# Performance work log

Measured on AMD Instinct MI355X. Metric: run time of the kernel, lower is better.

## Reference

```python
import jax, jax.numpy as jnp
import numpy as np

EPS = 1e-12  # guard sqrt at zero


def setup_inputs() -> dict:
    key = jax.random.key(0)
    k1, k2, k3 = jax.random.split(key, 3)
    B, N = 16, 2048
    pred_points = jax.random.normal(k1, (B, N, 3), dtype=jnp.float32)
    target_points = jax.random.normal(k2, (B, N, 3), dtype=jnp.float32)
    # binary symmetry flag per object, kept float for the blend
    sym_flag = (jax.random.uniform(k3, (B,)) > 0.5).astype(jnp.float32)
    return {"pred_points": pred_points, "target_points": target_points, "sym_flag": sym_flag}


def reference(pred_points, target_points, sym_flag):
    # Chamfer (ADD-S style): per pred point, min Euclidean distance to any target point.
    # Pairwise squared distances via ||p||^2 + ||t||^2 - 2 p.t  -> [B, N, M]
    p2 = jnp.sum(pred_points * pred_points, axis=-1)[:, :, None]   # [B,N,1]
    t2 = jnp.sum(target_points * target_points, axis=-1)[:, None, :]  # [B,1,M]
    cross = jnp.einsum('bnd,bmd->bnm', pred_points, target_points)  # [B,N,M]
    d2 = p2 + t2 - 2.0 * cross
    dist = jnp.sqrt(jnp.maximum(d2, EPS))                           # [B,N,M]
    sym_dis = jnp.min(dist, axis=2).mean(axis=1)                    # [B]

    # L2 (ADD style): per-point correspondence distance.
    asym_dis = jnp.linalg.norm(pred_points - target_points, axis=2).mean(axis=1)  # [B]

    all_loss = sym_flag * sym_dis + (1.0 - sym_flag) * asym_dis
    return all_loss.mean()
```

## Files before the change

### kernel.cpp

```cpp
#include <hip/hip_runtime.h>
#include <hip/hip_bf16.h>
#include <math.h>


typedef short short8 __attribute__((ext_vector_type(8)));
typedef float f32x16 __attribute__((ext_vector_type(16)));

__device__ __forceinline__ unsigned short f2bf(float f) {
  unsigned u = __float_as_uint(f);
  u = u + 0x7FFFu + ((u >> 16) & 1u);
  return (unsigned short)(u >> 16);
}
__device__ __forceinline__ float bf2f(unsigned short h) {
  return __uint_as_float(((unsigned)h) << 16);
}

#define TPB 256
#define NPTS 2048

__global__ __launch_bounds__(TPB, 2) void chamfer_main_kernel(
    const float* __restrict__ pred, const float* __restrict__ targ,
    const float* __restrict__ sym_flag, float* __restrict__ partial,
    int N, int B, int panelsPerBatch) {
  __shared__ short8 sA[2][NPTS];
  __shared__ float sm[4][64];

  const int blk = blockIdx.x;
  const int pp = blk % panelsPerBatch;
  const int b = blk / panelsPerBatch;

  const float* tb = targ + (size_t)b * N * 3;
  for (int t = threadIdx.x; t < NPTS; t += TPB) {
    const float x = tb[t * 3], y = tb[t * 3 + 1], z = tb[t * 3 + 2];
    const unsigned short thx = f2bf(x), thy = f2bf(y), thz = f2bf(z);
    const unsigned short tlx = f2bf(x - bf2f(thx));
    const unsigned short tly = f2bf(y - bf2f(thy));
    const unsigned short tlz = f2bf(z - bf2f(thz));
    const float q = 0.5f * (x * x + y * y + z * z);
    const unsigned short qh = f2bf(q), ql = f2bf(q - bf2f(qh));
    sA[0][t] = short8{(short)thx, (short)thy, (short)thz, (short)thx,
                      (short)thy, (short)thz, (short)tlx, (short)tly};
    sA[1][t] = short8{(short)tlz, (short)qh, (short)ql, 0, 0, 0, 0, 0};
  }

  const int lane = threadIdx.x & 63;
  const int w = threadIdx.x >> 6;
  const int g = lane >> 5;
  const int l31 = lane & 31;
  const int colBase = pp * 64;

  short8 bf0, bf1;
#pragma unroll
  for (int pt = 0; pt < 2; ++pt) {
    const int col = colBase + pt * 32 + l31;
    const float* pq = pred + ((size_t)b * N + col) * 3;
    const float x = pq[0], y = pq[1], z = pq[2];
    const unsigned short hx = f2bf(-x), hy = f2bf(-y), hz = f2bf(-z);
    const unsigned short lx = f2bf(-x - bf2f(hx));
    const unsigned short ly = f2bf(-y - bf2f(hy));
    const unsigned short lz = f2bf(-z - bf2f(hz));
    short8 r;
    if (g == 0)
      r = short8{(short)hx, (short)hy, (short)hz, (short)lx,
                 (short)ly, (short)lz, (short)hx, (short)hy};
    else
      r = short8{(short)hz, (short)0x3F80, (short)0x3F80, 0, 0, 0, 0, 0};
    if (pt == 0) bf0 = r; else bf1 = r;
  }
  __syncthreads();

  const f32x16 zc = {0.f, 0.f, 0.f, 0.f, 0.f, 0.f, 0.f, 0.f,
                     0.f, 0.f, 0.f, 0.f, 0.f, 0.f, 0.f, 0.f};
  float rm0[8], rm1[8];
#pragma unroll
  for (int i = 0; i < 8; ++i) { rm0[i] = 3.4e38f; rm1[i] = 3.4e38f; }

#pragma unroll 4
  for (int ta = 0; ta < 16; ++ta) {
    const short8 a = sA[g][w * 512 + ta * 32 + l31];
    const f32x16 d0 = __builtin_amdgcn_mfma_f32_32x32x16_bf16(a, bf0, zc, 0, 0, 0);
    const f32x16 d1 = __builtin_amdgcn_mfma_f32_32x32x16_bf16(a, bf1, zc, 0, 0, 0);
#pragma unroll
    for (int i = 0; i < 8; ++i) {
      rm0[i] = fminf(rm0[i], fminf(d0[2 * i], d0[2 * i + 1]));
      rm1[i] = fminf(rm1[i], fminf(d1[2 * i], d1[2 * i + 1]));
    }
  }

  float m0 = rm0[0], m1 = rm1[0];
#pragma unroll
  for (int i = 1; i < 8; ++i) { m0 = fminf(m0, rm0[i]); m1 = fminf(m1, rm1[i]); }
  m0 = fminf(m0, __shfl_xor(m0, 32));
  m1 = fminf(m1, __shfl_xor(m1, 32));
  if (lane < 32) {
    sm[w][l31] = m0;
    sm[w][32 + l31] = m1;
  }
  __syncthreads();

  if (threadIdx.x < 64) {
    const int i = threadIdx.x;
    const float mm = fminf(fminf(sm[0][i], sm[1][i]), fminf(sm[2][i], sm[3][i]));
    const size_t gc = (size_t)b * N + colBase + i;
    const float x = pred[gc * 3], y = pred[gc * 3 + 1], z = pred[gc * 3 + 2];
    const float tx = targ[gc * 3], ty = targ[gc * 3 + 1], tz = targ[gc * 3 + 2];
    const float hp2 = 0.5f * (x * x + y * y + z * z);
    const float dsym = sqrtf(fmaxf(2.f * (mm + hp2), 1e-12f));
    const float dx = x - tx, dy = y - ty, dz = z - tz;
    const float dasym = sqrtf(dx * dx + dy * dy + dz * dz);
    const float f = sym_flag[b];
    float c = f * dsym + (1.f - f) * dasym;
#pragma unroll
    for (int off = 32; off > 0; off >>= 1) c += __shfl_xor(c, off);
    if (i == 0) partial[blk] = c;
  }
}

__global__ __launch_bounds__(256) void chamfer_sum_kernel(
    const float* __restrict__ partial, float* __restrict__ out, float invNB) {
  const int t = threadIdx.x;
  float s = partial[t] + partial[t + 256];
#pragma unroll
  for (int off = 32; off > 0; off >>= 1) s += __shfl_xor(s, off);
  __shared__ float sW[4];
  if ((t & 63) == 0) sW[t >> 6] = s;
  __syncthreads();
  if (t == 0) out[0] = (sW[0] + sW[1] + sW[2] + sW[3]) * invNB;
}

extern "C" void kernel_launch(void* const* d_in, const int* in_sizes, int n_in,
                              void* d_out, int out_size, void* d_ws, size_t ws_size,
                              hipStream_t stream) {
  const float* pred = (const float*)d_in[0];
  const float* targ = (const float*)d_in[1];
  const float* sym_flag = (const float*)d_in[2];
  float* out = (float*)d_out;

  const int B = in_sizes[2];
  const int N = in_sizes[0] / (B * 3);

  const int panelsPerBatch = N / 64;
  const int grid = B * panelsPerBatch;
  float* partial = (float*)d_ws;

  chamfer_main_kernel<<<grid, TPB, 0, stream>>>(pred, targ, sym_flag, partial,
                                                N, B, panelsPerBatch);
  chamfer_sum_kernel<<<1, 256, 0, stream>>>(partial, out,
                                            1.0f / (float)(N * B));
}
```

Measured before the change: 14.86 us.

## Stage target points per wave with vector loads and drop the block barrier

Each wave now loads and converts only the 512 target points it later consumes, using float4 global loads of eight points per lane. This removes the block-wide __syncthreads between staging and the MFMA loop. The second shared-memory half is shrunk from short8 to short4, cutting LDS use from about 64KB to about 48KB. In exchange, the inner loop has a half-wave branch between the two LDS arrays plus vector repacking, and correctness relies on each wave reading only the region it wrote.

```diff
diff --git a/kernel.cpp b/kernel.cpp
--- a/kernel.cpp
+++ b/kernel.cpp
@@ -4,6 +4,7 @@
 
 
 typedef short short8 __attribute__((ext_vector_type(8)));
+typedef short short4v __attribute__((ext_vector_type(4)));
 typedef float f32x16 __attribute__((ext_vector_type(16)));
 
 __device__ __forceinline__ unsigned short f2bf(float f) {
@@ -22,26 +23,13 @@
     const float* __restrict__ pred, const float* __restrict__ targ,
     const float* __restrict__ sym_flag, float* __restrict__ partial,
     int N, int B, int panelsPerBatch) {
-  __shared__ short8 sA[2][NPTS];
+  __shared__ short8 sA0[NPTS];
+  __shared__ short4v sA1[NPTS];
   __shared__ float sm[4][64];
 
   const int blk = blockIdx.x;
   const int pp = blk % panelsPerBatch;
   const int b = blk / panelsPerBatch;
-
-  const float* tb = targ + (size_t)b * N * 3;
-  for (int t = threadIdx.x; t < NPTS; t += TPB) {
-    const float x = tb[t * 3], y = tb[t * 3 + 1], z = tb[t * 3 + 2];
-    const unsigned short thx = f2bf(x), thy = f2bf(y), thz = f2bf(z);
-    const unsigned short tlx = f2bf(x - bf2f(thx));
-    const unsigned short tly = f2bf(y - bf2f(thy));
-    const unsigned short tlz = f2bf(z - bf2f(thz));
-    const float q = 0.5f * (x * x + y * y + z * z);
-    const unsigned short qh = f2bf(q), ql = f2bf(q - bf2f(qh));
-    sA[0][t] = short8{(short)thx, (short)thy, (short)thz, (short)thx,
-                      (short)thy, (short)thz, (short)tlx, (short)tly};
-    sA[1][t] = short8{(short)tlz, (short)qh, (short)ql, 0, 0, 0, 0, 0};
-  }
 
   const int lane = threadIdx.x & 63;
   const int w = threadIdx.x >> 6;
@@ -67,7 +55,31 @@
       r = short8{(short)hz, (short)0x3F80, (short)0x3F80, 0, 0, 0, 0, 0};
     if (pt == 0) bf0 = r; else bf1 = r;
   }
-  __syncthreads();
+
+  {
+    const int t0 = w * 512 + lane * 8;
+    const float4* tg4 = (const float4*)(targ + ((size_t)b * N + t0) * 3);
+    float tf[24];
+#pragma unroll
+    for (int k = 0; k < 6; ++k) {
+      const float4 v = tg4[k];
+      tf[4 * k] = v.x; tf[4 * k + 1] = v.y;
+      tf[4 * k + 2] = v.z; tf[4 * k + 3] = v.w;
+    }
+#pragma unroll
+    for (int j = 0; j < 8; ++j) {
+      const float x = tf[3 * j], y = tf[3 * j + 1], z = tf[3 * j + 2];
+      const unsigned short thx = f2bf(x), thy = f2bf(y), thz = f2bf(z);
+      const unsigned short tlx = f2bf(x - bf2f(thx));
+      const unsigned short tly = f2bf(y - bf2f(thy));
+      const unsigned short tlz = f2bf(z - bf2f(thz));
+      const float q = 0.5f * fmaf(z, z, fmaf(y, y, x * x));
+      const unsigned short qh = f2bf(q), ql = f2bf(q - bf2f(qh));
+      sA0[t0 + j] = short8{(short)thx, (short)thy, (short)thz, (short)thx,
+                           (short)thy, (short)thz, (short)tlx, (short)tly};
+      sA1[t0 + j] = short4v{(short)tlz, (short)qh, (short)ql, 0};
+    }
+  }
 
   const f32x16 zc = {0.f, 0.f, 0.f, 0.f, 0.f, 0.f, 0.f, 0.f,
                      0.f, 0.f, 0.f, 0.f, 0.f, 0.f, 0.f, 0.f};
@@ -77,7 +89,14 @@
 
 #pragma unroll 4
   for (int ta = 0; ta < 16; ++ta) {
-    const short8 a = sA[g][w * 512 + ta * 32 + l31];
+    const int idx = w * 512 + ta * 32 + l31;
+    short8 a;
+    if (g == 0) {
+      a = sA0[idx];
+    } else {
+      const short4v v = sA1[idx];
+      a = short8{v.x, v.y, v.z, v.w, 0, 0, 0, 0};
+    }
     const f32x16 d0 = __builtin_amdgcn_mfma_f32_32x32x16_bf16(a, bf0, zc, 0, 0, 0);
     const f32x16 d1 = __builtin_amdgcn_mfma_f32_32x32x16_bf16(a, bf1, zc, 0, 0, 0);
 #pragma unroll
```

Result: slower. 15.23 us (+2.5%).
